# Performance work log

Measured on AMD Instinct MI355X. Metric: run time of the kernel, lower is better.

Reference implementation:

```python
import jax, jax.numpy as jnp
import numpy as np

B, T, C, H = 4, 2048, 1024, 16
D = C // H


def setup_inputs() -> dict:
    key = jax.random.key(0)
    ks = jax.random.split(key, 6)
    s = 1.0 / np.sqrt(C)
    return {
        "x": jax.random.normal(ks[0], (B, T, C), dtype=jnp.float32),
        "attention_mask": jnp.ones((B, 1, T), dtype=jnp.int32),
        "Wq": jax.random.normal(ks[1], (C, C), dtype=jnp.float32) * s,
        "bq": jnp.zeros((C,), dtype=jnp.float32),
        "Wk": jax.random.normal(ks[2], (C, C), dtype=jnp.float32) * s,
        "bk": jnp.zeros((C,), dtype=jnp.float32),
        "Wv": jax.random.normal(ks[3], (C, C), dtype=jnp.float32) * s,
        "bv": jnp.zeros((C,), dtype=jnp.float32),
        "Wp": jax.random.normal(ks[4], (C, C), dtype=jnp.float32) * s,
        "bp": jnp.zeros((C,), dtype=jnp.float32),
    }


def reference(x, attention_mask, Wq, bq, Wk, bk, Wv, bv, Wp, bp):
    b, t, c = x.shape
    d = c // H
    # projections (torch Linear: x @ W^T + b)
    q = (x @ Wq.T + bq).reshape(b, t, H, d).transpose(0, 2, 1, 3)  # [B,H,T,D]
    k = (x @ Wk.T + bk).reshape(b, t, H, d).transpose(0, 2, 1, 3)
    v = (x @ Wv.T + bv).reshape(b, t, H, d).transpose(0, 2, 1, 3)
    attn = jnp.einsum("bhqd,bhkd->bhqk", q, k) / jnp.sqrt(jnp.asarray(d, x.dtype))
    mask = attention_mask[:, :, :t]  # [B,1,T] -> broadcast over [B,H,T,T] keys
    attn = jnp.where(mask[:, :, None, :] == 0, jnp.asarray(-jnp.inf, x.dtype), attn)
    attn = jax.nn.softmax(attn, axis=-1)  # dropout p=0 (eval)
    y = jnp.einsum("bhqk,bhkd->bhqd", attn, v)
    y = y.transpose(0, 2, 1, 3).reshape(b, t, c)
    return y @ Wp.T + bp
```

## Files before the change

### kernel.cpp

```cpp
#include <hip/hip_runtime.h>


#define TT 2048
#define CC 1024
#define HH 16
#define DD 64
#define BB 4

typedef unsigned short u16;
typedef unsigned int u32;
typedef __attribute__((ext_vector_type(8))) short bf16x8;
typedef __attribute__((ext_vector_type(4))) float f32x4;
typedef __attribute__((ext_vector_type(4))) u32 u32x4;

#if __has_builtin(__builtin_amdgcn_exp2f)
#define EXP2(x) __builtin_amdgcn_exp2f(x)
#else
#define EXP2(x) __expf((x) * 0.6931471805599453f)
#endif

__device__ __forceinline__ u16 f2bf(float f) {
    u32 u = __builtin_bit_cast(u32, f);
    u += 0x7FFFu + ((u >> 16) & 1u);
    return (u16)(u >> 16);
}
__device__ __forceinline__ u32 pk2(float a, float b) {
    u32 ua = __builtin_bit_cast(u32, a); ua += 0x7FFFu + ((ua >> 16) & 1u);
    u32 ub = __builtin_bit_cast(u32, b); ub += 0x7FFFu + ((ub >> 16) & 1u);
    return __builtin_amdgcn_perm(ub, ua, 0x07060302);
}
__device__ __forceinline__ u32 cvtpk(float lo, float hi) {
    u32 r;
    asm("v_cvt_pk_bf16_f32 %0, %1, %2" : "=v"(r) : "v"(lo), "v"(hi));
    return r;
}

#define GLDS(g, l) __builtin_amdgcn_global_load_lds( \
    (const __attribute__((address_space(1))) void*)(g), \
    (__attribute__((address_space(3))) void*)(l), 16, 0, 0)

__global__ __launch_bounds__(256) void wcvt(const float* __restrict__ s,
                                            u16* __restrict__ d, int n8) {
    const int i = blockIdx.x * 256 + threadIdx.x;
    if (i < n8) {
        const float4 f0 = ((const float4*)s)[2 * i];
        const float4 f1 = ((const float4*)s)[2 * i + 1];
        uint4 w;
        w.x = pk2(f0.x, f0.y); w.y = pk2(f0.z, f0.w);
        w.z = pk2(f1.x, f1.y); w.w = pk2(f1.z, f1.w);
        ((uint4*)d)[i] = w;
    }
}

__global__ __launch_bounds__(256) void wcvt3(const float* __restrict__ s0,
                                             const float* __restrict__ s1,
                                             const float* __restrict__ s2,
                                             u16* __restrict__ d0,
                                             u16* __restrict__ d1,
                                             u16* __restrict__ d2, int n8) {
    const int which = blockIdx.y;
    const float* s = (which == 0) ? s0 : (which == 1) ? s1 : s2;
    u16* d = (which == 0) ? d0 : (which == 1) ? d1 : d2;
    const int i = blockIdx.x * 256 + threadIdx.x;
    if (i < n8) {
        const float4 f0 = ((const float4*)s)[2 * i];
        const float4 f1 = ((const float4*)s)[2 * i + 1];
        uint4 w;
        w.x = pk2(f0.x, f0.y); w.y = pk2(f0.z, f0.w);
        w.z = pk2(f1.x, f1.y); w.w = pk2(f1.z, f1.w);
        ((uint4*)d)[i] = w;
    }
}

template <int PROJ>
__global__ __launch_bounds__(256) void gemmX(const u16* __restrict__ A,
                                             const u16* __restrict__ Wb,
                                             const float* __restrict__ b0,
                                             const float* __restrict__ b1,
                                             const float* __restrict__ b2,
                                             void* __restrict__ out0,
                                             void* __restrict__ out1,
                                             void* __restrict__ out2) {
    __shared__ u16 As[128 * 64];
    __shared__ u16 Bs[128 * 64];

    const int tid  = threadIdx.x;
    const int wave = tid >> 6, lane = tid & 63;
    const int quad = lane >> 4, l16 = lane & 15;
    const int bm = blockIdx.y * 128, bn = blockIdx.x * 128;
    const int wm = (wave >> 1) * 64, wn = (wave & 1) * 64;
    const int K = CC;

    f32x4 acc[4][4] = {};

    for (int k0 = 0; k0 < K; k0 += 64) {
#pragma unroll
        for (int rr = 0; rr < 4; rr++) {
            const int c = rr * 256 + tid;
            const int row = c >> 3;
            const int cs = ((c & 7) ^ (row & 7)) * 8;
            GLDS(&Wb[(size_t)(bn + row) * K + k0 + cs], &Bs[c * 8]);
        }
#pragma unroll
        for (int rr = 0; rr < 4; rr++) {
            const int c = rr * 256 + tid;
            const int row = c >> 3;
            const int cs = ((c & 7) ^ (row & 7)) * 8;
            GLDS(&A[(size_t)(bm + row) * K + k0 + cs], &As[c * 8]);
        }
        __syncthreads();

#pragma unroll
        for (int ks = 0; ks < 2; ks++) {
            bf16x8 af[4], bfr[4];
#pragma unroll
            for (int i = 0; i < 4; i++) {
                const int row = wm + i * 16 + l16;
                const int s8 = (ks * 4 + quad) ^ (row & 7);
                af[i] = *(bf16x8*)&As[row * 64 + s8 * 8];
            }
#pragma unroll
            for (int j = 0; j < 4; j++) {
                const int row = wn + j * 16 + l16;
                const int s8 = (ks * 4 + quad) ^ (row & 7);
                bfr[j] = *(bf16x8*)&Bs[row * 64 + s8 * 8];
            }
#pragma unroll
            for (int i = 0; i < 4; i++)
#pragma unroll
                for (int j = 0; j < 4; j++)
                    acc[i][j] = __builtin_amdgcn_mfma_f32_16x16x32_bf16(af[i], bfr[j], acc[i][j], 0, 0, 0);
        }
        __syncthreads();
    }

    if (PROJ) {
        float* out = (float*)out0;
#pragma unroll
        for (int j = 0; j < 4; j++) {
            const int col = bn + wn + j * 16 + l16;
            const float bv = b0[col];
#pragma unroll
            for (int i = 0; i < 4; i++) {
                const int row0 = bm + wm + i * 16 + quad * 4;
#pragma unroll
                for (int r = 0; r < 4; r++)
                    out[(size_t)(row0 + r) * CC + col] = acc[i][j][r] + bv;
            }
        }
    } else {
        const int mid = bn >> 10;
        const float* bias = (mid == 0) ? b0 : (mid == 1) ? b1 : b2;
#pragma unroll
        for (int j = 0; j < 4; j++) {
            const int col  = bn + wn + j * 16 + l16;
            const int colL = col & (CC - 1);
            const float bv = bias[colL];
#pragma unroll
            for (int i = 0; i < 4; i++) {
                const int row0 = bm + wm + i * 16 + quad * 4;
                if (mid < 2) {
                    u16* out = (u16*)(mid ? out1 : out0);
#pragma unroll
                    for (int r = 0; r < 4; r++)
                        out[(size_t)(row0 + r) * CC + colL] = f2bf(acc[i][j][r] + bv);
                } else {
                    const int hh = colL >> 6, dch = colL & 63;
                    const int bb = row0 >> 11, t0 = row0 & (TT - 1);
                    const size_t idx = (((size_t)bb * HH + hh) * DD + dch) * TT + t0;
                    uint2 w;
                    w.x = pk2(acc[i][j][0] + bv, acc[i][j][1] + bv);
                    w.y = pk2(acc[i][j][2] + bv, acc[i][j][3] + bv);
                    *(uint2*)&((u16*)out2)[idx] = w;
                }
            }
        }
    }
}

__global__ __launch_bounds__(256) void attn(const u16* __restrict__ Q,
                                            const u16* __restrict__ Kb,
                                            const u16* __restrict__ Vt,
                                            const int* __restrict__ mask,
                                            u16* __restrict__ Y) {
    const int b = blockIdx.z, h = blockIdx.y, qt = blockIdx.x;
    const int tid  = threadIdx.x;
    const int wave = tid >> 6, lane = tid & 63;
    const int quad = lane >> 4, l16 = lane & 15;
    const int qrow0 = qt * 128 + wave * 32;

    __shared__ u16 Ks[2][64 * 64];
    __shared__ u16 Vs[2][64 * 64];
    __shared__ __align__(16) float bias_lds[TT];

    const size_t qb = ((size_t)b * TT + qrow0) * CC + h * DD;

    bf16x8 qf[2][2];
#pragma unroll
    for (int m = 0; m < 2; m++)
#pragma unroll
        for (int ks = 0; ks < 2; ks++)
            qf[m][ks] = *(const bf16x8*)&Q[qb + (size_t)(m * 16 + l16) * CC + ks * 32 + quad * 8];

    {
        const int i = tid * 8;
        const int4 m0 = *(const int4*)&mask[b * TT + i];
        const int4 m1 = *(const int4*)&mask[b * TT + i + 4];
        bias_lds[i + 0] = m0.x ? 0.f : -1e38f;
        bias_lds[i + 1] = m0.y ? 0.f : -1e38f;
        bias_lds[i + 2] = m0.z ? 0.f : -1e38f;
        bias_lds[i + 3] = m0.w ? 0.f : -1e38f;
        bias_lds[i + 4] = m1.x ? 0.f : -1e38f;
        bias_lds[i + 5] = m1.y ? 0.f : -1e38f;
        bias_lds[i + 6] = m1.z ? 0.f : -1e38f;
        bias_lds[i + 7] = m1.w ? 0.f : -1e38f;
    }

    const int c0 = tid, c1 = tid + 256;
    const int r0 = c0 >> 3, r1 = c1 >> 3;
    const int kp0 = (c0 & 7) ^ ((((r0 >> 3) & 1) << 2) | (r0 & 3));
    const int kp1 = (c1 & 7) ^ ((((r1 >> 3) & 1) << 2) | (r1 & 3));
    const int vp0 = (c0 & 7) ^ (r0 & 7), vp1 = (c1 & 7) ^ (r1 & 7);
    const u16* kgp = Kb + ((size_t)b * TT) * CC + h * DD;
    const u16* vgp = Vt + ((size_t)(b * HH + h) * DD) * TT;

    const int rowA = ((l16 >> 2) << 3) | (l16 & 3);
    const int s0k  = (((l16 >> 2) & 1) << 2) | (l16 & 3);

    f32x4 o[2][4] = {};
    float lsum[2] = {};
    const float SC = 0.18033688011112042f;

    GLDS(&kgp[(size_t)r0 * CC + kp0 * 8], &Ks[0][c0 * 8]);
    GLDS(&kgp[(size_t)r1 * CC + kp1 * 8], &Ks[0][c1 * 8]);
    GLDS(&vgp[(size_t)r0 * TT + vp0 * 8], &Vs[0][c0 * 8]);
    GLDS(&vgp[(size_t)r1 * TT + vp1 * 8], &Vs[0][c1 * 8]);
    asm volatile("s_waitcnt vmcnt(0) lgkmcnt(0)" ::: "memory");
    __builtin_amdgcn_s_barrier();
    __builtin_amdgcn_sched_barrier(0);

#pragma unroll 1
    for (int kt = 0; kt < TT; kt += 64) {
        const int cur = (kt >> 6) & 1;
        const u16* Kc = &Ks[cur][0];
        const u16* Vc = &Vs[cur][0];

        if (kt + 64 < TT) {
            const int nxt = cur ^ 1;
            GLDS(&kgp[(size_t)(kt + 64 + r0) * CC + kp0 * 8], &Ks[nxt][c0 * 8]);
            GLDS(&kgp[(size_t)(kt + 64 + r1) * CC + kp1 * 8], &Ks[nxt][c1 * 8]);
            GLDS(&vgp[(size_t)r0 * TT + kt + 64 + vp0 * 8], &Vs[nxt][c0 * 8]);
            GLDS(&vgp[(size_t)r1 * TT + kt + 64 + vp1 * 8], &Vs[nxt][c1 * 8]);
        }

        const f32x4 bA = *(const f32x4*)&bias_lds[kt + quad * 8];
        const f32x4 bB = *(const f32x4*)&bias_lds[kt + quad * 8 + 4];
        const f32x4 bC = *(const f32x4*)&bias_lds[kt + 32 + quad * 8];
        const f32x4 bD = *(const f32x4*)&bias_lds[kt + 32 + quad * 8 + 4];

        f32x4 s2[2][4] = {};
        __builtin_amdgcn_s_setprio(1);
#pragma unroll
        for (int n = 0; n < 4; n++) {
            const int rowK = rowA + (n & 1) * 4 + (n >> 1) * 32;
#pragma unroll
            for (int ks = 0; ks < 2; ks++) {
                const int pos = ((ks << 2) + quad) ^ s0k;
                const bf16x8 kf = *(const bf16x8*)&Kc[rowK * 64 + pos * 8];
#pragma unroll
                for (int m = 0; m < 2; m++)
                    s2[m][n] = __builtin_amdgcn_mfma_f32_16x16x32_bf16(kf, qf[m][ks], s2[m][n], 0, 0, 0);
            }
        }
        __builtin_amdgcn_s_setprio(0);

        u32 pkk[2][8];
#pragma unroll
        for (int m = 0; m < 2; m++) {
            float ls = 0.f;
#pragma unroll
            for (int n = 0; n < 4; n++) {
                const f32x4 bv = (n == 0) ? bA : (n == 1) ? bB : (n == 2) ? bC : bD;
                const float p0 = EXP2(fmaf(s2[m][n][0], SC, bv[0]));
                const float p1 = EXP2(fmaf(s2[m][n][1], SC, bv[1]));
                const float p2 = EXP2(fmaf(s2[m][n][2], SC, bv[2]));
                const float p3 = EXP2(fmaf(s2[m][n][3], SC, bv[3]));
                ls += (p0 + p1) + (p2 + p3);
                pkk[m][2 * n]     = cvtpk(p0, p1);
                pkk[m][2 * n + 1] = cvtpk(p2, p3);
            }
            lsum[m] += ls;
        }

        __builtin_amdgcn_s_setprio(1);
#pragma unroll
        for (int ks = 0; ks < 2; ks++) {
            bf16x8 pf[2];
#pragma unroll
            for (int m = 0; m < 2; m++) {
                const u32x4 t = { pkk[m][4 * ks + 0], pkk[m][4 * ks + 1],
                                  pkk[m][4 * ks + 2], pkk[m][4 * ks + 3] };
                pf[m] = __builtin_bit_cast(bf16x8, t);
            }
#pragma unroll
            for (int dt = 0; dt < 4; dt++) {
                const int vrow = dt * 16 + l16;
                const int pos = ((ks << 2) + quad) ^ (vrow & 7);
                const bf16x8 vf = *(const bf16x8*)&Vc[vrow * 64 + pos * 8];
#pragma unroll
                for (int m = 0; m < 2; m++)
                    o[m][dt] = __builtin_amdgcn_mfma_f32_16x16x32_bf16(pf[m], vf, o[m][dt], 0, 0, 0);
            }
        }
        __builtin_amdgcn_s_setprio(0);

        asm volatile("s_waitcnt vmcnt(0)" ::: "memory");
        __builtin_amdgcn_sched_barrier(0);
        __builtin_amdgcn_s_barrier();
    }

#pragma unroll
    for (int m = 0; m < 2; m++) {
        lsum[m] += __shfl_xor(lsum[m], 16, 64);
        lsum[m] += __shfl_xor(lsum[m], 32, 64);
    }

#pragma unroll
    for (int m = 0; m < 2; m++) {
        float inv[4];
#pragma unroll
        for (int r = 0; r < 4; r++)
            inv[r] = 1.0f / __shfl(lsum[m], quad * 4 + r, 64);
#pragma unroll
        for (int dt = 0; dt < 4; dt++)
#pragma unroll
            for (int r = 0; r < 4; r++)
                Y[qb + (size_t)(m * 16 + quad * 4 + r) * CC + dt * 16 + l16] = f2bf(o[m][dt][r] * inv[r]);
    }
}

extern "C" void kernel_launch(void* const* d_in, const int* in_sizes, int n_in,
                              void* d_out, int out_size, void* d_ws, size_t ws_size,
                              hipStream_t stream) {
    const float* x    = (const float*)d_in[0];
    const int*   mask = (const int*)d_in[1];
    const float* Wq   = (const float*)d_in[2];
    const float* bq   = (const float*)d_in[3];
    const float* Wk   = (const float*)d_in[4];
    const float* bk   = (const float*)d_in[5];
    const float* Wv   = (const float*)d_in[6];
    const float* bv   = (const float*)d_in[7];
    const float* Wp   = (const float*)d_in[8];
    const float* bp   = (const float*)d_in[9];

    u16* ws = (u16*)d_ws;
    const size_t sz = (size_t)BB * TT * CC;
    u16* Qb   = ws;
    u16* Kbuf = ws + sz;
    u16* Vtb  = ws + 2 * sz;

    u16* xb   = (u16*)d_out;
    u16* Wq16 = xb + sz;
    u16* Wk16 = Wq16 + (size_t)CC * CC;
    u16* Wv16 = Wk16 + (size_t)CC * CC;

    const int W8 = CC * CC / 8;
    wcvt<<<4096, 256, 0, stream>>>(x, xb, (int)(sz / 8));
    wcvt3<<<dim3(512, 3), 256, 0, stream>>>(Wq, Wk, Wv, Wq16, Wk16, Wv16, W8);

    gemmX<0><<<dim3(24, 64), 256, 0, stream>>>(xb, Wq16, bq, bk, bv, Qb, Kbuf, Vtb);

    attn<<<dim3(TT / 128, HH, BB), 256, 0, stream>>>(Qb, Kbuf, Vtb, mask, Qb);

    wcvt<<<512, 256, 0, stream>>>(Wp, Kbuf, W8);
    gemmX<1><<<dim3(8, 64), 256, 0, stream>>>(Qb, Kbuf, bp, nullptr, nullptr, d_out, nullptr, nullptr);
}
```

Measured before the change: 312.1 us.

## Double attention block to 8 waves over 256 queries and interleave softmax with PV

The attention kernel now runs 512 threads per block, each covering 256 query rows. Every K/V tile loaded into LDS is therefore shared by twice as many waves, and each thread issues half as many global-to-LDS loads. The exp/pack work is split per ks half so that softmax for the second half can overlap the PV MFMAs of the first, with priority raised only around the MFMAs. The cost is fewer blocks (512 instead of 1024) and more waves waiting on each barrier.

Measured after the change: 289.5 us. 7.2% less time.

```diff
diff --git a/kernel.cpp b/kernel.cpp
--- a/kernel.cpp
+++ b/kernel.cpp
@@ -178,7 +178,7 @@
     }
 }
 
-__global__ __launch_bounds__(256) void attn(const u16* __restrict__ Q,
+__global__ __launch_bounds__(512) void attn(const u16* __restrict__ Q,
                                             const u16* __restrict__ Kb,
                                             const u16* __restrict__ Vt,
                                             const int* __restrict__ mask,
@@ -187,7 +187,7 @@
     const int tid  = threadIdx.x;
     const int wave = tid >> 6, lane = tid & 63;
     const int quad = lane >> 4, l16 = lane & 15;
-    const int qrow0 = qt * 128 + wave * 32;
+    const int qrow0 = qt * 256 + wave * 32;
 
     __shared__ u16 Ks[2][64 * 64];
     __shared__ u16 Vs[2][64 * 64];
@@ -203,24 +203,18 @@
             qf[m][ks] = *(const bf16x8*)&Q[qb + (size_t)(m * 16 + l16) * CC + ks * 32 + quad * 8];
 
     {
-        const int i = tid * 8;
+        const int i = tid * 4;
         const int4 m0 = *(const int4*)&mask[b * TT + i];
-        const int4 m1 = *(const int4*)&mask[b * TT + i + 4];
         bias_lds[i + 0] = m0.x ? 0.f : -1e38f;
         bias_lds[i + 1] = m0.y ? 0.f : -1e38f;
         bias_lds[i + 2] = m0.z ? 0.f : -1e38f;
         bias_lds[i + 3] = m0.w ? 0.f : -1e38f;
-        bias_lds[i + 4] = m1.x ? 0.f : -1e38f;
-        bias_lds[i + 5] = m1.y ? 0.f : -1e38f;
-        bias_lds[i + 6] = m1.z ? 0.f : -1e38f;
-        bias_lds[i + 7] = m1.w ? 0.f : -1e38f;
-    }
-
-    const int c0 = tid, c1 = tid + 256;
-    const int r0 = c0 >> 3, r1 = c1 >> 3;
+    }
+
+    const int c0 = tid;
+    const int r0 = c0 >> 3;
     const int kp0 = (c0 & 7) ^ ((((r0 >> 3) & 1) << 2) | (r0 & 3));
-    const int kp1 = (c1 & 7) ^ ((((r1 >> 3) & 1) << 2) | (r1 & 3));
-    const int vp0 = (c0 & 7) ^ (r0 & 7), vp1 = (c1 & 7) ^ (r1 & 7);
+    const int vp0 = (c0 & 7) ^ (r0 & 7);
     const u16* kgp = Kb + ((size_t)b * TT) * CC + h * DD;
     const u16* vgp = Vt + ((size_t)(b * HH + h) * DD) * TT;
 
@@ -232,9 +226,7 @@
     const float SC = 0.18033688011112042f;
 
     GLDS(&kgp[(size_t)r0 * CC + kp0 * 8], &Ks[0][c0 * 8]);
-    GLDS(&kgp[(size_t)r1 * CC + kp1 * 8], &Ks[0][c1 * 8]);
     GLDS(&vgp[(size_t)r0 * TT + vp0 * 8], &Vs[0][c0 * 8]);
-    GLDS(&vgp[(size_t)r1 * TT + vp1 * 8], &Vs[0][c1 * 8]);
     asm volatile("s_waitcnt vmcnt(0) lgkmcnt(0)" ::: "memory");
     __builtin_amdgcn_s_barrier();
     __builtin_amdgcn_sched_barrier(0);
@@ -248,9 +240,7 @@
         if (kt + 64 < TT) {
             const int nxt = cur ^ 1;
             GLDS(&kgp[(size_t)(kt + 64 + r0) * CC + kp0 * 8], &Ks[nxt][c0 * 8]);
-            GLDS(&kgp[(size_t)(kt + 64 + r1) * CC + kp1 * 8], &Ks[nxt][c1 * 8]);
             GLDS(&vgp[(size_t)r0 * TT + kt + 64 + vp0 * 8], &Vs[nxt][c0 * 8]);
-            GLDS(&vgp[(size_t)r1 * TT + kt + 64 + vp1 * 8], &Vs[nxt][c1 * 8]);
         }
 
         const f32x4 bA = *(const f32x4*)&bias_lds[kt + quad * 8];
@@ -274,34 +264,28 @@
         }
         __builtin_amdgcn_s_setprio(0);
 
-        u32 pkk[2][8];
-#pragma unroll
-        for (int m = 0; m < 2; m++) {
-            float ls = 0.f;
-#pragma unroll
-            for (int n = 0; n < 4; n++) {
-                const f32x4 bv = (n == 0) ? bA : (n == 1) ? bB : (n == 2) ? bC : bD;
-                const float p0 = EXP2(fmaf(s2[m][n][0], SC, bv[0]));
-                const float p1 = EXP2(fmaf(s2[m][n][1], SC, bv[1]));
-                const float p2 = EXP2(fmaf(s2[m][n][2], SC, bv[2]));
-                const float p3 = EXP2(fmaf(s2[m][n][3], SC, bv[3]));
-                ls += (p0 + p1) + (p2 + p3);
-                pkk[m][2 * n]     = cvtpk(p0, p1);
-                pkk[m][2 * n + 1] = cvtpk(p2, p3);
-            }
-            lsum[m] += ls;
-        }
-
-        __builtin_amdgcn_s_setprio(1);
 #pragma unroll
         for (int ks = 0; ks < 2; ks++) {
             bf16x8 pf[2];
 #pragma unroll
             for (int m = 0; m < 2; m++) {
-                const u32x4 t = { pkk[m][4 * ks + 0], pkk[m][4 * ks + 1],
-                                  pkk[m][4 * ks + 2], pkk[m][4 * ks + 3] };
+                u32 pw[4];
+#pragma unroll
+                for (int nn = 0; nn < 2; nn++) {
+                    const int n = 2 * ks + nn;
+                    const f32x4 bv = (n == 0) ? bA : (n == 1) ? bB : (n == 2) ? bC : bD;
+                    const float p0 = EXP2(fmaf(s2[m][n][0], SC, bv[0]));
+                    const float p1 = EXP2(fmaf(s2[m][n][1], SC, bv[1]));
+                    const float p2 = EXP2(fmaf(s2[m][n][2], SC, bv[2]));
+                    const float p3 = EXP2(fmaf(s2[m][n][3], SC, bv[3]));
+                    lsum[m] += (p0 + p1) + (p2 + p3);
+                    pw[2 * nn]     = cvtpk(p0, p1);
+                    pw[2 * nn + 1] = cvtpk(p2, p3);
+                }
+                const u32x4 t = { pw[0], pw[1], pw[2], pw[3] };
                 pf[m] = __builtin_bit_cast(bf16x8, t);
             }
+            __builtin_amdgcn_s_setprio(1);
 #pragma unroll
             for (int dt = 0; dt < 4; dt++) {
                 const int vrow = dt * 16 + l16;
@@ -311,8 +295,8 @@
                 for (int m = 0; m < 2; m++)
                     o[m][dt] = __builtin_amdgcn_mfma_f32_16x16x32_bf16(pf[m], vf, o[m][dt], 0, 0, 0);
             }
-        }
-        __builtin_amdgcn_s_setprio(0);
+            __builtin_amdgcn_s_setprio(0);
+        }
 
         asm volatile("s_waitcnt vmcnt(0)" ::: "memory");
         __builtin_amdgcn_sched_barrier(0);
@@ -370,7 +354,7 @@
 
     gemmX<0><<<dim3(24, 64), 256, 0, stream>>>(xb, Wq16, bq, bk, bv, Qb, Kbuf, Vtb);
 
-    attn<<<dim3(TT / 128, HH, BB), 256, 0, stream>>>(Qb, Kbuf, Vtb, mask, Qb);
+    attn<<<dim3(TT / 256, HH, BB), 512, 0, stream>>>(Qb, Kbuf, Vtb, mask, Qb);
 
     wcvt<<<512, 256, 0, stream>>>(Wp, Kbuf, W8);
     gemmX<1><<<dim3(8, 64), 256, 0, stream>>>(Qb, Kbuf, bp, nullptr, nullptr, d_out, nullptr, nullptr);
```
